# Kernel optimization log

Measured on AMD Instinct MI355X. Metric: run time of the kernel, lower is better.

## Reference

```python
import jax, jax.numpy as jnp
import numpy as np

H, HKV, D = 8, 1, 256  # query heads, kv heads, head_dim (Gemma-2B-like)


def apply_rope(x, sin, cos):
    # x: [B, h, D, S]; sin/cos: [B, 1, D//2, S]
    x1, x2 = jnp.split(x, 2, axis=-2)
    return jnp.concatenate((x1 * cos - x2 * sin, x2 * cos + x1 * sin), axis=-2)


def setup_inputs() -> dict:
    key = jax.random.key(0)
    ks = jax.random.split(key, 12)
    B, hidden, S = 2, 2048, 2048
    half = D // 2
    Xq = jax.random.normal(ks[0], (B, hidden, S), jnp.float32)
    Xkv = jax.random.normal(ks[1], (B, hidden, S), jnp.float32)
    sin_q = jax.random.uniform(ks[2], (B, 1, half, S), jnp.float32, -1.0, 1.0)
    cos_q = jax.random.uniform(ks[3], (B, 1, half, S), jnp.float32, -1.0, 1.0)
    sin_k = jax.random.uniform(ks[4], (B, 1, half, S), jnp.float32, -1.0, 1.0)
    cos_k = jax.random.uniform(ks[5], (B, 1, half, S), jnp.float32, -1.0, 1.0)
    attn_mask = jnp.zeros((B, 1, S, S), jnp.float32)
    scale = 0.02
    Wq = jax.random.normal(ks[6], (H * D, hidden), jnp.float32) * scale
    Wk = jax.random.normal(ks[7], (HKV * D, hidden), jnp.float32) * scale
    Wv = jax.random.normal(ks[8], (HKV * D, hidden), jnp.float32) * scale
    Wo = jax.random.normal(ks[9], (hidden, H * D), jnp.float32) * scale
    return {"Xq": Xq, "Xkv": Xkv, "sin_q": sin_q, "cos_q": cos_q,
            "sin_k": sin_k, "cos_k": cos_k, "attn_mask": attn_mask,
            "Wq": Wq, "Wk": Wk, "Wv": Wv, "Wo": Wo}


def reference(Xq, Xkv, sin_q, cos_q, sin_k, cos_k, attn_mask, Wq, Wk, Wv, Wo):
    B, hidden, Sq = Xq.shape
    Sk = Xkv.shape[-1]
    # ANEDenseGeneral = 1x1 conv over channels-first layout
    q = jnp.einsum('oc,bcs->bos', Wq, Xq).reshape(B, H, D, Sq)
    q = apply_rope(q, sin_q, cos_q)
    k = jnp.einsum('oc,bcs->bos', Wk, Xkv).reshape(B, HKV, D, Sk)
    k = apply_rope(k, sin_k, cos_k)
    v = jnp.einsum('oc,bcs->bos', Wv, Xkv).reshape(B, HKV, D, Sk)
    # GQA: broadcast kv heads to query heads
    rep = H // HKV
    k = jnp.repeat(k, rep, axis=1)
    v = jnp.repeat(v, rep, axis=1)
    scale = 1.0 / jnp.sqrt(jnp.asarray(D, Xq.dtype))
    scores = jnp.einsum('bhdq,bhdk->bhqk', q, k) * scale + attn_mask
    probs = jax.nn.softmax(scores, axis=-1)
    out = jnp.einsum('bhqk,bhdk->bhdq', probs, v).reshape(B, H * D, Sq)
    return jnp.einsum('oc,bcs->bos', Wo, out).astype(Xq.dtype)
```

## Files before the change

kernel.cpp:

```cpp
#include <hip/hip_runtime.h>

typedef __bf16 bf16;
typedef __bf16 bf16x8 __attribute__((ext_vector_type(8)));
typedef __bf16 bf16x4 __attribute__((ext_vector_type(4)));
typedef __bf16 bf16x2 __attribute__((ext_vector_type(2)));
typedef float f32x4 __attribute__((ext_vector_type(4)));
typedef float f32x16 __attribute__((ext_vector_type(16)));
typedef unsigned u32;
typedef unsigned u32x4v __attribute__((ext_vector_type(4)));

static constexpr int Hh = 8;
static constexpr int Dd = 256;
static constexpr int Ss = 2048;
static constexpr int Cc = 2048;

typedef const __attribute__((address_space(1))) unsigned int as1_u32;
typedef __attribute__((address_space(3))) unsigned int as3_u32;

__device__ __forceinline__ void gl_lds16(const void* g, void* l) {
  __builtin_amdgcn_global_load_lds((as1_u32*)(unsigned long long)g,
                                   (as3_u32*)(unsigned int)(unsigned long long)l,
                                   16, 0, 0);
}

__device__ __forceinline__ f32x4 mfma16(bf16x8 a, bf16x8 b, f32x4 c) {
  return __builtin_amdgcn_mfma_f32_16x16x32_bf16(a, b, c, 0, 0, 0);
}
__device__ __forceinline__ f32x16 mfma32(bf16x8 a, bf16x8 b, f32x16 c) {
  return __builtin_amdgcn_mfma_f32_32x32x16_bf16(a, b, c, 0, 0, 0);
}

__device__ __forceinline__ u32 pk_bf16(float lo, float hi) {
  bf16x2 t;
  t[0] = (bf16)lo;
  t[1] = (bf16)hi;
  return __builtin_bit_cast(u32, t);
}

__global__ __launch_bounds__(256) void cvt_w(const float* __restrict__ in,
                                             bf16* __restrict__ out, int n) {
  int i = (blockIdx.x * 256 + threadIdx.x) * 4;
  if (i >= n) return;
  const float4 v = *(const float4*)(in + i);
  bf16x4 o;
  o[0] = (bf16)v.x; o[1] = (bf16)v.y; o[2] = (bf16)v.z; o[3] = (bf16)v.w;
  *(bf16x4*)(out + i) = o;
}

__global__ __launch_bounds__(256) void transpose_cvt(const float* __restrict__ in,
                                                     bf16* __restrict__ out,
                                                     int R, int S) {
  __shared__ float t[32][33];
  const int b = blockIdx.z;
  const long base = (long)b * R * S;
  const int s0 = blockIdx.x * 32, r0 = blockIdx.y * 32;
  const int tx = threadIdx.x, ty = threadIdx.y;
#pragma unroll
  for (int i = 0; i < 32; i += 8)
    t[ty + i][tx] = in[base + (long)(r0 + ty + i) * S + s0 + tx];
  __syncthreads();
#pragma unroll
  for (int i = 0; i < 32; i += 8)
    out[base + (long)(s0 + ty + i) * R + r0 + tx] = (bf16)t[tx][ty + i];
}

__global__ __launch_bounds__(256) void rope_transpose(
    const bf16* __restrict__ xin, const bf16* __restrict__ sint,
    const bf16* __restrict__ cost, bf16* __restrict__ xout, int nH,
    long bStr) {
  __shared__ __align__(16) bf16 ti[32][264];
  const int b = blockIdx.z, h = blockIdx.y, s0 = blockIdx.x * 32;
  const int tx = threadIdx.x, ty = threadIdx.y;
  const bf16* src = xin + (long)b * bStr + (long)h * Dd * Ss + s0;
#pragma unroll
  for (int i = 0; i < 32; ++i) {
    int d = ty + i * 8;
    ti[tx][d] = src[(long)d * Ss + tx];
  }
  __syncthreads();
  const int t = ty * 32 + tx;
  const int s = t >> 3;
  const int dpart = t & 7;
  const bf16* sp = sint + ((long)b * Ss + s0 + s) * 128;
  const bf16* cp = cost + ((long)b * Ss + s0 + s) * 128;
  bf16* dst = xout + (((long)(b * nH + h)) * Ss + s0 + s) * Dd;
#pragma unroll
  for (int i = 0; i < 4; ++i) {
    int d0 = dpart * 8 + i * 64;
    int dh = d0 & 127;
    bf16x8 a = *(const bf16x8*)&ti[s][d0];
    bf16x8 p = *(const bf16x8*)&ti[s][(d0 < 128) ? d0 + 128 : d0 - 128];
    bf16x8 sn = *(const bf16x8*)&sp[dh];
    bf16x8 cs = *(const bf16x8*)&cp[dh];
    bf16x8 o;
#pragma unroll
    for (int j = 0; j < 8; ++j) {
      float av = (float)a[j], pv = (float)p[j];
      float c = (float)cs[j], sv = (float)sn[j];
      float val = (d0 < 128) ? (av * c - pv * sv) : (av * c + pv * sv);
      o[j] = (bf16)val;
    }
    *(bf16x8*)&dst[d0] = o;
  }
}

__global__ __launch_bounds__(256, 2) void gemm_bt(
    const bf16* __restrict__ A, const bf16* __restrict__ Bt,
    bf16* __restrict__ Cb, float* __restrict__ Cf, int M, int N, int K,
    long sBt, long sC) {
  __shared__ __align__(16) bf16 lA[2][128 * 64];
  __shared__ __align__(16) bf16 lB[2][128 * 64];
  const int tid = threadIdx.x;
  const int wid = tid >> 6, lane = tid & 63;
  const int g = lane >> 4, r = lane & 15;
  const int wr = wid >> 1, wc = wid & 1;
  const int mt = blockIdx.y * 128, nt = blockIdx.x * 128;
  const int z = blockIdx.z;
  const bf16* Bz = Bt + (long)z * sBt;

  auto stage = [&](int buf, int kt) {
#pragma unroll
    for (int it = 0; it < 4; ++it) {
      int off = it * 4096 + tid * 16;
      int row = off >> 7;
      int c = (off >> 4) & 7;
      int csw = c ^ (row & 7);
      gl_lds16((const char*)(A + (long)(mt + row) * K + kt) + csw * 16,
               (char*)lA[buf] + it * 4096 + wid * 1024);
      gl_lds16((const char*)(Bz + (long)(nt + row) * K + kt) + csw * 16,
               (char*)lB[buf] + it * 4096 + wid * 1024);
    }
  };

  const f32x4 zf = {0.f, 0.f, 0.f, 0.f};
  f32x4 acc[4][4];
#pragma unroll
  for (int m = 0; m < 4; ++m)
#pragma unroll
    for (int n = 0; n < 4; ++n) acc[m][n] = zf;

  stage(0, 0);
  __syncthreads();
  int cur = 0;
  for (int kt = 0; kt < K; kt += 64) {
    if (kt + 64 < K) stage(cur ^ 1, kt + 64);
#pragma unroll
    for (int kk = 0; kk < 2; ++kk) {
      bf16x8 af[4], bfv[4];
#pragma unroll
      for (int m = 0; m < 4; ++m) {
        int row = wr * 64 + m * 16 + r;
        int csw = (kk * 4 + g) ^ (row & 7);
        af[m] = *(const bf16x8*)((const char*)lA[cur] + row * 128 + csw * 16);
      }
#pragma unroll
      for (int n = 0; n < 4; ++n) {
        int row = wc * 64 + n * 16 + r;
        int csw = (kk * 4 + g) ^ (row & 7);
        bfv[n] = *(const bf16x8*)((const char*)lB[cur] + row * 128 + csw * 16);
      }
#pragma unroll
      for (int m = 0; m < 4; ++m)
#pragma unroll
        for (int n = 0; n < 4; ++n)
          acc[m][n] = mfma16(af[m], bfv[n], acc[m][n]);
    }
    __syncthreads();
    cur ^= 1;
  }

#pragma unroll
  for (int m = 0; m < 4; ++m)
#pragma unroll
    for (int n = 0; n < 4; ++n)
#pragma unroll
      for (int e = 0; e < 4; ++e) {
        int orow = mt + wr * 64 + m * 16 + g * 4 + e;
        int col = nt + wc * 64 + n * 16 + r;
        long idx = (long)z * sC + (long)orow * N + col;
        if (Cf) Cf[idx] = acc[m][n][e];
        else Cb[idx] = (bf16)acc[m][n][e];
      }
}

__global__ __launch_bounds__(256, 1) void attn_kernel(
    const bf16* __restrict__ qr, const bf16* __restrict__ kr,
    const bf16* __restrict__ kv, const float* __restrict__ mask,
    bf16* __restrict__ aout) {
  __shared__ __align__(16) bf16 lK[2][32 * 256];
  __shared__ __align__(16) bf16 lV[2][256 * 32];
  const int i = blockIdx.x;
  const int flat = (i & 7) * 32 + (i >> 3);
  const int b = flat >> 7;
  const int hg = (flat >> 6) & 1;
  const int q0 = (flat & 63) * 32;
  const int tid = threadIdx.x;
  const int wid = tid >> 6, lane = tid & 63;
  const int l31 = lane & 31, hi = lane >> 5;
  const int h = hg * 4 + wid;

  bf16x8 qf[16];
  const bf16* qp = qr + (((long)(b * Hh + h)) * Ss + q0 + l31) * Dd;
#pragma unroll
  for (int kk = 0; kk < 16; ++kk)
    qf[kk] = *(const bf16x8*)&qp[kk * 16 + hi * 8];

  f32x16 oacc[8] = {};
  float mrun = -3e38f, lrun = 0.f;

  const char* kb = (const char*)(kr + (long)b * Ss * Dd);
  const char* vb = (const char*)(kv + ((long)b * 2 * Dd + Dd) * Ss);
  const float* mb = mask + (long)b * Ss * Ss;

  auto stage = [&](int buf, int kt) {
    const char* gK = kb + (long)kt * 512;
#pragma unroll
    for (int it = 0; it < 4; ++it) {
      int off = it * 4096 + tid * 16;
      int row = off >> 9;
      int c = (off >> 4) & 31;
      int csw = c ^ (row & 7);
      gl_lds16(gK + row * 512 + csw * 16,
               (char*)lK[buf] + it * 4096 + wid * 1024);
    }
#pragma unroll
    for (int it = 0; it < 4; ++it) {
      int off = it * 4096 + tid * 16;
      int row = off >> 6;
      int c = (off >> 4) & 3;
      int csw = c ^ ((row >> 1) & 3);
      gl_lds16(vb + (long)row * (Ss * 2) + (long)kt * 2 + csw * 16,
               (char*)lV[buf] + it * 4096 + wid * 1024);
    }
  };

  stage(0, 0);
  __syncthreads();
  int cur = 0;

  for (int kt = 0; kt < Ss; kt += 32) {
    if (kt + 32 < Ss) stage(cur ^ 1, kt + 32);

    const float* mrow = mb + (long)(q0 + l31) * Ss + kt;
    float4 mv[4];
#pragma unroll
    for (int grp = 0; grp < 4; ++grp)
      mv[grp] = *(const float4*)(mrow + grp * 8 + hi * 4);

    f32x16 sacc = {};
    __builtin_amdgcn_s_setprio(1);
#pragma unroll
    for (int kk = 0; kk < 16; ++kk) {
      int csw = (kk * 2 + hi) ^ (l31 & 7);
      bf16x8 kf = *(const bf16x8*)((const char*)lK[cur] + l31 * 512 + csw * 16);
      sacc = mfma32(kf, qf[kk], sacc);
    }
    __builtin_amdgcn_s_setprio(0);

    float x[16];
#pragma unroll
    for (int r = 0; r < 16; ++r)
      x[r] = sacc[r] * 0.0625f + ((const float*)&mv[r >> 2])[r & 3];
    float mx = x[0];
#pragma unroll
    for (int r = 1; r < 16; ++r) mx = fmaxf(mx, x[r]);
    mx = fmaxf(mx, __shfl_xor(mx, 32, 64));
    if (mx > mrun + 8.0f) {
      float al = __expf(mrun - mx);
      lrun *= al;
#pragma unroll
      for (int d = 0; d < 8; ++d) oacc[d] *= al;
      mrun = mx;
    }
    float p[16];
    float rs = 0.f;
#pragma unroll
    for (int r = 0; r < 16; ++r) {
      p[r] = __expf(x[r] - mrun);
      rs += p[r];
    }
    rs += __shfl_xor(rs, 32, 64);
    lrun += rs;

    bf16x8 pf[2];
#pragma unroll
    for (int kk2 = 0; kk2 < 2; ++kk2) {
      u32 a0 = pk_bf16(p[kk2 * 8 + 0], p[kk2 * 8 + 1]);
      u32 a1 = pk_bf16(p[kk2 * 8 + 2], p[kk2 * 8 + 3]);
      u32 b0 = pk_bf16(p[kk2 * 8 + 4], p[kk2 * 8 + 5]);
      u32 b1 = pk_bf16(p[kk2 * 8 + 6], p[kk2 * 8 + 7]);
      asm("v_permlane32_swap_b32 %0, %1" : "+v"(a0), "+v"(b0));
      asm("v_permlane32_swap_b32 %0, %1" : "+v"(a1), "+v"(b1));
      u32x4v w;
      w[0] = a0; w[1] = a1; w[2] = b0; w[3] = b1;
      pf[kk2] = __builtin_bit_cast(bf16x8, w);
    }

    __builtin_amdgcn_s_setprio(1);
#pragma unroll
    for (int kk2 = 0; kk2 < 2; ++kk2) {
#pragma unroll
      for (int db = 0; db < 8; ++db) {
        int csw = (kk2 * 2 + hi) ^ ((l31 >> 1) & 3);
        bf16x8 vf = *(const bf16x8*)((const char*)lV[cur] +
                                     (db * 32 + l31) * 64 + csw * 16);
        oacc[db] = mfma32(vf, pf[kk2], oacc[db]);
      }
    }
    __builtin_amdgcn_s_setprio(0);

    __syncthreads();
    cur ^= 1;
  }

  const float inv = 1.f / lrun;
  bf16* op = aout + ((long)(b * Ss + q0 + l31)) * (Hh * Dd) + h * Dd;
#pragma unroll
  for (int db = 0; db < 8; ++db) {
#pragma unroll
    for (int grp = 0; grp < 4; ++grp) {
      bf16x4 o4;
#pragma unroll
      for (int e = 0; e < 4; ++e) o4[e] = (bf16)(oacc[db][grp * 4 + e] * inv);
      *(bf16x4*)&op[db * 32 + grp * 8 + hi * 4] = o4;
    }
  }
}

extern "C" void kernel_launch(void* const* d_in, const int* in_sizes, int n_in,
                              void* d_out, int out_size, void* d_ws,
                              size_t ws_size, hipStream_t stream) {
  const float* Xq = (const float*)d_in[0];
  const float* Xkv = (const float*)d_in[1];
  const float* sin_q = (const float*)d_in[2];
  const float* cos_q = (const float*)d_in[3];
  const float* sin_k = (const float*)d_in[4];
  const float* cos_k = (const float*)d_in[5];
  const float* mask = (const float*)d_in[6];
  const float* Wq = (const float*)d_in[7];
  const float* Wk = (const float*)d_in[8];
  const float* Wv = (const float*)d_in[9];
  const float* Wo = (const float*)d_in[10];
  float* out = (float*)d_out;

  char* ws = (char*)d_ws;
  const size_t MB = 1u << 20;
  bf16* Wq_bf = (bf16*)(ws + 0 * MB);
  bf16* Wo_bf = (bf16*)(ws + 8 * MB);
  bf16* Wkv_bf = (bf16*)(ws + 16 * MB);
  bf16* Wv_bf = (bf16*)(ws + 17 * MB);
  bf16* sin_qt = (bf16*)(ws + 18 * MB);
  bf16* cos_qt = (bf16*)(ws + 19 * MB);
  bf16* sin_kt = (bf16*)(ws + 20 * MB);
  bf16* cos_kt = (bf16*)(ws + 21 * MB);
  bf16* Xtq = (bf16*)(ws + 22 * MB);
  bf16* Xtkv = (bf16*)(ws + 38 * MB);
  bf16* q_tmp = (bf16*)(ws + 54 * MB);
  bf16* kv_tmp = (bf16*)(ws + 70 * MB);
  bf16* qr = (bf16*)(ws + 22 * MB);
  bf16* kr = (bf16*)(ws + 38 * MB);
  bf16* attnb = (bf16*)(ws + 54 * MB);

  dim3 b256(256), b32x8(32, 8);

  cvt_w<<<4096, b256, 0, stream>>>(Wq, Wq_bf, Cc * Cc);
  cvt_w<<<4096, b256, 0, stream>>>(Wo, Wo_bf, Cc * Cc);
  cvt_w<<<512, b256, 0, stream>>>(Wk, (bf16*)Wkv_bf, Dd * Cc);
  cvt_w<<<512, b256, 0, stream>>>(Wv, Wv_bf, Dd * Cc);

  transpose_cvt<<<dim3(64, 64, 2), b32x8, 0, stream>>>(Xq, Xtq, Cc, Ss);
  transpose_cvt<<<dim3(64, 64, 2), b32x8, 0, stream>>>(Xkv, Xtkv, Cc, Ss);
  transpose_cvt<<<dim3(64, 4, 2), b32x8, 0, stream>>>(sin_q, sin_qt, 128, Ss);
  transpose_cvt<<<dim3(64, 4, 2), b32x8, 0, stream>>>(cos_q, cos_qt, 128, Ss);
  transpose_cvt<<<dim3(64, 4, 2), b32x8, 0, stream>>>(sin_k, sin_kt, 128, Ss);
  transpose_cvt<<<dim3(64, 4, 2), b32x8, 0, stream>>>(cos_k, cos_kt, 128, Ss);

  gemm_bt<<<dim3(16, 16, 2), b256, 0, stream>>>(
      Wq_bf, Xtq, q_tmp, nullptr, Cc, Ss, Cc, (long)Ss * Cc, (long)Cc * Ss);
  gemm_bt<<<dim3(16, 4, 2), b256, 0, stream>>>(
      Wkv_bf, Xtkv, kv_tmp, nullptr, 2 * Dd, Ss, Cc, (long)Ss * Cc,
      (long)2 * Dd * Ss);

  rope_transpose<<<dim3(64, 8, 2), b32x8, 0, stream>>>(
      q_tmp, sin_qt, cos_qt, qr, Hh, (long)Hh * Dd * Ss);
  rope_transpose<<<dim3(64, 1, 2), b32x8, 0, stream>>>(
      kv_tmp, sin_kt, cos_kt, kr, 1, (long)2 * Dd * Ss);

  attn_kernel<<<dim3(256), b256, 0, stream>>>(qr, kr, kv_tmp, mask, attnb);

  gemm_bt<<<dim3(16, 16, 2), b256, 0, stream>>>(
      Wo_bf, attnb, nullptr, out, Cc, Ss, Cc, (long)Ss * Cc, (long)Cc * Ss);
}
```

Baseline: 307.6 us.

## Split attention key range across two wave groups and merge partial softmax

```diff
diff --git a/kernel.cpp b/kernel.cpp
--- a/kernel.cpp
+++ b/kernel.cpp
@@ -183,12 +183,16 @@
       }
 }
 
-__global__ __launch_bounds__(256, 1) void attn_kernel(
+__global__ __launch_bounds__(512, 2) void attn_kernel(
     const bf16* __restrict__ qr, const bf16* __restrict__ kr,
     const bf16* __restrict__ kv, const float* __restrict__ mask,
     bf16* __restrict__ aout) {
-  __shared__ __align__(16) bf16 lK[2][32 * 256];
-  __shared__ __align__(16) bf16 lV[2][256 * 32];
+  __shared__ __align__(16) char smem[131072];
+  __shared__ float mbuf[4][64], lbuf[4][64];
+  auto lKp = [&](int kvh, int buf) { return smem + (kvh * 2 + buf) * 16384; };
+  auto lVp = [&](int kvh, int buf) {
+    return smem + 65536 + (kvh * 2 + buf) * 16384;
+  };
   const int i = blockIdx.x;
   const int flat = (i & 7) * 32 + (i >> 3);
   const int b = flat >> 7;
@@ -197,7 +201,10 @@
   const int tid = threadIdx.x;
   const int wid = tid >> 6, lane = tid & 63;
   const int l31 = lane & 31, hi = lane >> 5;
-  const int h = hg * 4 + wid;
+  const int h = hg * 4 + (wid & 3);
+  const int kvh = wid >> 2;
+  const int ht = tid & 255;
+  const int hwid = (tid >> 6) & 3;
 
   bf16x8 qf[16];
   const bf16* qp = qr + (((long)(b * Hh + h)) * Ss + q0 + l31) * Dd;
@@ -214,32 +221,36 @@
 
   auto stage = [&](int buf, int kt) {
     const char* gK = kb + (long)kt * 512;
+    char* LK = lKp(kvh, buf);
+    char* LV = lVp(kvh, buf);
 #pragma unroll
     for (int it = 0; it < 4; ++it) {
-      int off = it * 4096 + tid * 16;
+      int off = it * 4096 + ht * 16;
       int row = off >> 9;
       int c = (off >> 4) & 31;
       int csw = c ^ (row & 7);
-      gl_lds16(gK + row * 512 + csw * 16,
-               (char*)lK[buf] + it * 4096 + wid * 1024);
+      gl_lds16(gK + row * 512 + csw * 16, LK + it * 4096 + hwid * 1024);
     }
 #pragma unroll
     for (int it = 0; it < 4; ++it) {
-      int off = it * 4096 + tid * 16;
+      int off = it * 4096 + ht * 16;
       int row = off >> 6;
       int c = (off >> 4) & 3;
       int csw = c ^ ((row >> 1) & 3);
       gl_lds16(vb + (long)row * (Ss * 2) + (long)kt * 2 + csw * 16,
-               (char*)lV[buf] + it * 4096 + wid * 1024);
+               LV + it * 4096 + hwid * 1024);
     }
   };
 
-  stage(0, 0);
+  const int kbeg = kvh * (Ss / 2), kend = kbeg + (Ss / 2);
+  stage(0, kbeg);
   __syncthreads();
   int cur = 0;
 
-  for (int kt = 0; kt < Ss; kt += 32) {
-    if (kt + 32 < Ss) stage(cur ^ 1, kt + 32);
+  for (int kt = kbeg; kt < kend; kt += 32) {
+    if (kt + 32 < kend) stage(cur ^ 1, kt + 32);
+    const char* LK = lKp(kvh, cur);
+    const char* LV = lVp(kvh, cur);
 
     const float* mrow = mb + (long)(q0 + l31) * Ss + kt;
     float4 mv[4];
@@ -252,7 +263,7 @@
 #pragma unroll
     for (int kk = 0; kk < 16; ++kk) {
       int csw = (kk * 2 + hi) ^ (l31 & 7);
-      bf16x8 kf = *(const bf16x8*)((const char*)lK[cur] + l31 * 512 + csw * 16);
+      bf16x8 kf = *(const bf16x8*)(LK + l31 * 512 + csw * 16);
       sacc = mfma32(kf, qf[kk], sacc);
     }
     __builtin_amdgcn_s_setprio(0);
@@ -302,8 +313,7 @@
 #pragma unroll
       for (int db = 0; db < 8; ++db) {
         int csw = (kk2 * 2 + hi) ^ ((l31 >> 1) & 3);
-        bf16x8 vf = *(const bf16x8*)((const char*)lV[cur] +
-                                     (db * 32 + l31) * 64 + csw * 16);
+        bf16x8 vf = *(const bf16x8*)(LV + (db * 32 + l31) * 64 + csw * 16);
         oacc[db] = mfma32(vf, pf[kk2], oacc[db]);
       }
     }
@@ -313,16 +323,40 @@
     cur ^= 1;
   }
 
-  const float inv = 1.f / lrun;
-  bf16* op = aout + ((long)(b * Ss + q0 + l31)) * (Hh * Dd) + h * Dd;
-#pragma unroll
-  for (int db = 0; db < 8; ++db) {
-#pragma unroll
-    for (int grp = 0; grp < 4; ++grp) {
-      bf16x4 o4;
-#pragma unroll
-      for (int e = 0; e < 4; ++e) o4[e] = (bf16)(oacc[db][grp * 4 + e] * inv);
-      *(bf16x4*)&op[db * 32 + grp * 8 + hi * 4] = o4;
+  float* dump = (float*)smem;
+  if (wid >= 4) {
+    float* base = dump + (wid - 4) * 8192;
+#pragma unroll
+    for (int db = 0; db < 8; ++db)
+#pragma unroll
+      for (int grp = 0; grp < 4; ++grp) {
+        f32x4 c;
+#pragma unroll
+        for (int e = 0; e < 4; ++e) c[e] = oacc[db][grp * 4 + e];
+        *(f32x4*)&base[db * 1024 + grp * 256 + lane * 4] = c;
+      }
+    mbuf[wid - 4][lane] = mrun;
+    lbuf[wid - 4][lane] = lrun;
+  }
+  __syncthreads();
+  if (wid < 4) {
+    const float* base = dump + wid * 8192;
+    float m1 = mbuf[wid][lane], l1 = lbuf[wid][lane];
+    float m = fmaxf(mrun, m1);
+    float a0 = __expf(mrun - m), a1 = __expf(m1 - m);
+    const float inv = 1.f / (lrun * a0 + l1 * a1);
+    bf16* op = aout + ((long)(b * Ss + q0 + l31)) * (Hh * Dd) + h * Dd;
+#pragma unroll
+    for (int db = 0; db < 8; ++db) {
+#pragma unroll
+      for (int grp = 0; grp < 4; ++grp) {
+        f32x4 t = *(const f32x4*)&base[db * 1024 + grp * 256 + lane * 4];
+        bf16x4 o4;
+#pragma unroll
+        for (int e = 0; e < 4; ++e)
+          o4[e] = (bf16)((oacc[db][grp * 4 + e] * a0 + t[e] * a1) * inv);
+        *(bf16x4*)&op[db * 32 + grp * 8 + hi * 4] = o4;
+      }
     }
   }
 }
@@ -386,7 +420,8 @@
   rope_transpose<<<dim3(64, 1, 2), b32x8, 0, stream>>>(
       kv_tmp, sin_kt, cos_kt, kr, 1, (long)2 * Dd * Ss);
 
-  attn_kernel<<<dim3(256), b256, 0, stream>>>(qr, kr, kv_tmp, mask, attnb);
+  attn_kernel<<<dim3(256), dim3(512), 0, stream>>>(qr, kr, kv_tmp, mask,
+                                                   attnb);
 
   gemm_bt<<<dim3(16, 16, 2), b256, 0, stream>>>(
       Wo_bf, attnb, nullptr, out, Cc, Ss, Cc, (long)Ss * Cc, (long)Cc * Ss);
```

Result: no change. 304.4 us (-1.0%).
